# Kernel optimization log

Hardware: AMD Instinct MI355X
Metric: run time of the kernel (lower is better)

The kernel has to match this reference:

```python
import jax, jax.numpy as jnp
import numpy as np

S_Q = 2048; B = 2; H = 16; D = 128
SCALE = 1.0 / np.sqrt(128.0)  # softmax_scale from init


def setup_inputs() -> dict:
    key = jax.random.key(0)
    kq, kk, kv, ks = jax.random.split(key, 4)
    q = jax.random.normal(kq, (S_Q, B, H, D), dtype=jnp.float32)
    k = jax.random.normal(kk, (S_Q, B, 1, D), dtype=jnp.float32)   # MQA: H_kv=1
    v = jax.random.normal(kv, (S_Q, B, 1, D), dtype=jnp.float32)
    sinks = jax.random.normal(ks, (H,), dtype=jnp.float32)         # learned per-head sink logits
    return {"q": q, "k": k, "v": v, "sinks": sinks, "mask": 0}


def reference(q, k, v, sinks, mask):
    # q: [S_q, B, H, D]; k, v: [S_k, B, H_kv, D] (H_kv may be 1 -> MQA expand)
    S_q, Bn, Hq, Dn = q.shape
    S_k = k.shape[0]
    k = jnp.broadcast_to(k, (S_k, Bn, Hq, Dn))
    v = jnp.broadcast_to(v, (S_k, Bn, Hq, Dn))
    # logits: [B, H, S_q, S_k]
    logits = jnp.einsum("sbhd,tbhd->bhst", q.astype(jnp.float32), k.astype(jnp.float32)) * SCALE
    # causal mask (triu(-inf, diag=1) added in original)
    causal = jnp.tril(jnp.ones((S_q, S_k), dtype=bool))
    logits = jnp.where(causal[None, None], logits, -jnp.inf)
    # sink-augmented softmax: append sink logit as extra column, softmax, drop it
    sink = sinks.astype(jnp.float32)[None, :, None, None]        # [1, H, 1, 1]
    m = jax.lax.stop_gradient(jnp.maximum(logits.max(axis=-1, keepdims=True), sink))
    e = jnp.exp(logits - m)                                      # [B, H, S_q, S_k]
    denom = e.sum(axis=-1, keepdims=True) + jnp.exp(sink - m)    # sink column contribution
    probs = e / denom
    out = jnp.einsum("bhst,tbhd->sbhd", probs.astype(v.dtype), v)  # [S_q, B, H, D]
    return out.reshape(S_q, Bn, Hq * Dn)
```

## Files before the change

### kernel.cpp

```cpp
#include <hip/hip_runtime.h>
#include <hip/hip_bf16.h>

#define SQ 2048
#define NB 2
#define NH 16
#define DH 128
#define NKT 32
#define NQT 16
#define SCALE_L2E 0.1275174609f
#define LOG2E 1.4426950408889634f
#define DEFER_THR 11.0f

typedef _Float16 f16x8 __attribute__((ext_vector_type(8)));
typedef _Float16 f16x4 __attribute__((ext_vector_type(4)));
typedef __fp16 fp16x2 __attribute__((ext_vector_type(2)));
typedef float f32x4 __attribute__((ext_vector_type(4)));
typedef float f32x16 __attribute__((ext_vector_type(16)));
typedef unsigned int u32x4 __attribute__((ext_vector_type(4)));

static __device__ __forceinline__ _Float16 f2h(float f) { return (_Float16)f; }

static __device__ __forceinline__ unsigned int pkrtz(float a, float b) {
    fp16x2 h = __builtin_amdgcn_cvt_pkrtz(a, b);
    return __builtin_bit_cast(unsigned int, h);
}

__global__ __launch_bounds__(256)
void prepack(const float* __restrict__ k, const float* __restrict__ v,
             _Float16* __restrict__ kws, _Float16* __restrict__ vws) {
    const int tile  = blockIdx.x;
    const int which = tile >> 6;
    const int b     = (tile >> 5) & 1;
    const int kt    = tile & 31;
    const int tid   = threadIdx.x;

    if (which == 0) {
        const float* kbase = k + (size_t)kt * 64 * (NB * DH) + b * DH;
        _Float16* dst = kws + ((size_t)b * NKT + kt) * 8192;
        #pragma unroll
        for (int p = 0; p < 8; ++p) {
            const int id4 = tid + p * 256;
            const int row = id4 >> 5;
            const int c0  = (id4 & 31) << 2;
            f32x4 a = *(const f32x4*)(kbase + (size_t)row * (NB * DH) + c0);
            const int e = (row * 128 + c0) ^ ((row & 7) << 3);
            f16x4 pk = { f2h(a.x), f2h(a.y), f2h(a.z), f2h(a.w) };
            *(f16x4*)(dst + e) = pk;
        }
    } else {
        const float* vbase = v + b * DH;
        _Float16* dst = vws + ((size_t)b * NKT + kt) * 8192;
        const int d    = tid & 127;
        const int half = tid >> 7;
        #pragma unroll
        for (int p = 0; p < 8; ++p) {
            const int c0 = (p * 2 + half) * 4;
            float a0 = vbase[(size_t)(kt * 64 + c0 + 0) * (NB * DH) + d];
            float a1 = vbase[(size_t)(kt * 64 + c0 + 1) * (NB * DH) + d];
            float a2 = vbase[(size_t)(kt * 64 + c0 + 2) * (NB * DH) + d];
            float a3 = vbase[(size_t)(kt * 64 + c0 + 3) * (NB * DH) + d];
            const int e = (d * 64 + c0) ^ ((d & 7) << 3);
            f16x4 pk = { f2h(a0), f2h(a1), f2h(a2), f2h(a3) };
            *(f16x4*)(dst + e) = pk;
        }
    }
}

static __device__ __forceinline__ void gload16(const _Float16* gsrc, _Float16* ldst) {
    __builtin_amdgcn_global_load_lds(
        (const __attribute__((address_space(1))) void*)gsrc,
        (__attribute__((address_space(3))) void*)ldst, 16, 0, 0);
}

__global__ __launch_bounds__(256)
void attn_fwd(const float* __restrict__ q, const _Float16* __restrict__ kws,
              const _Float16* __restrict__ vws, const float* __restrict__ sinks,
              float* __restrict__ out) {
    __shared__ _Float16 Kb[2][8192];
    __shared__ _Float16 Vb[2][8192];

    const int tid  = threadIdx.x;
    const int w    = tid >> 6;
    const int lane = tid & 63;
    const int qc   = lane & 31;
    const int h2   = lane >> 5;

    const int bid  = blockIdx.x;
    const int b    = bid & 1;
    const int h    = (bid >> 1) & 15;
    const int slot = bid >> 5;
    const int qt   = (slot < 8) ? slot : 23 - slot;
    const int q0   = qt * 128;
    const int sq   = q0 + w * 32 + qc;

    f16x8 qf[8];
    {
        const float* qrow = q + ((size_t)sq * NB + b) * (NH * DH) + h * DH;
        #pragma unroll
        for (int ks = 0; ks < 8; ++ks) {
            const int d0 = ks * 16 + h2 * 8;
            f32x4 a = *(const f32x4*)(qrow + d0);
            f32x4 c = *(const f32x4*)(qrow + d0 + 4);
            f16x8 t;
            t[0] = f2h(a.x * SCALE_L2E); t[1] = f2h(a.y * SCALE_L2E);
            t[2] = f2h(a.z * SCALE_L2E); t[3] = f2h(a.w * SCALE_L2E);
            t[4] = f2h(c.x * SCALE_L2E); t[5] = f2h(c.y * SCALE_L2E);
            t[6] = f2h(c.z * SCALE_L2E); t[7] = f2h(c.w * SCALE_L2E);
            qf[ks] = t;
        }
    }

    float m_run = sinks[h] * LOG2E;
    float l_run = 1.0f;
    f32x16 acc[4];
    #pragma unroll
    for (int i = 0; i < 4; ++i) acc[i] = (f32x16)(0.0f);

    const _Float16* ktiles = kws + (size_t)b * NKT * 8192;
    const _Float16* vtiles = vws + (size_t)b * NKT * 8192;
    const int ntiles = 2 * qt + 2;

    #pragma unroll
    for (int j = 0; j < 4; ++j) {
        const int off = (w * 4 + j) * 512;
        gload16(ktiles + off + lane * 8, &Kb[0][off]);
        gload16(vtiles + off + lane * 8, &Vb[0][off]);
    }
    asm volatile("s_waitcnt vmcnt(0)" ::: "memory");
    __builtin_amdgcn_s_barrier();

    for (int it = 0; it < ntiles; ++it) {
        const int cur = it & 1;
        if (it + 1 < ntiles) {
            const _Float16* kt_n = ktiles + (size_t)(it + 1) * 8192;
            const _Float16* vt_n = vtiles + (size_t)(it + 1) * 8192;
            #pragma unroll
            for (int j = 0; j < 4; ++j) {
                const int off = (w * 4 + j) * 512;
                gload16(kt_n + off + lane * 8, &Kb[cur ^ 1][off]);
                gload16(vt_n + off + lane * 8, &Vb[cur ^ 1][off]);
            }
        }

        const int ktbase = it * 64;
        if (ktbase <= q0 + w * 32 + 31) {
            f32x16 sa0 = (f32x16)(0.0f), sa1 = (f32x16)(0.0f);
            __builtin_amdgcn_s_setprio(1);
            #pragma unroll
            for (int ks = 0; ks < 8; ++ks) {
                const int col = ks * 16 + h2 * 8;
                const int e0 = (qc * 128 + col) ^ ((qc & 7) << 3);
                const int e1 = ((32 + qc) * 128 + col) ^ ((qc & 7) << 3);
                f16x8 k0 = *(const f16x8*)(&Kb[cur][e0]);
                f16x8 k1 = *(const f16x8*)(&Kb[cur][e1]);
                sa0 = __builtin_amdgcn_mfma_f32_32x32x16_f16(k0, qf[ks], sa0, 0, 0, 0);
                sa1 = __builtin_amdgcn_mfma_f32_32x32x16_f16(k1, qf[ks], sa1, 0, 0, 0);
            }
            __builtin_amdgcn_s_setprio(0);

            float sv[32];
            #pragma unroll
            for (int i = 0; i < 16; ++i) { sv[i] = sa0[i]; sv[16 + i] = sa1[i]; }

            if (ktbase + 63 > q0 + w * 32) {
                #pragma unroll
                for (int mt = 0; mt < 2; ++mt)
                    #pragma unroll
                    for (int i = 0; i < 16; ++i) {
                        const int tk = ktbase + (i & 3) + 8 * (i >> 2) + 4 * h2 + 32 * mt;
                        if (tk > sq) sv[mt * 16 + i] = -1e30f;
                    }
            }

            float mx = sv[0];
            #pragma unroll
            for (int i = 1; i < 32; ++i) mx = fmaxf(mx, sv[i]);
            mx = fmaxf(mx, __shfl_xor(mx, 32));

            if (!__all(mx <= m_run + DEFER_THR)) {
                const float mnew = fmaxf(m_run, mx);
                const float corr = __builtin_amdgcn_exp2f(m_run - mnew);
                m_run = mnew;
                l_run *= corr;
                #pragma unroll
                for (int mt = 0; mt < 4; ++mt) acc[mt] *= corr;
            }

            float ls = 0.0f;
            #pragma unroll
            for (int i = 0; i < 32; ++i) {
                const float p = __builtin_amdgcn_exp2f(sv[i] - m_run);
                sv[i] = p;
                ls += p;
            }
            ls += __shfl_xor(ls, 32);
            l_run += ls;

            unsigned int pw[4][4];
            #pragma unroll
            for (int mt = 0; mt < 2; ++mt) {
                unsigned int e0[4], e1[4];
                #pragma unroll
                for (int bq = 0; bq < 4; ++bq) {
                    e0[bq] = pkrtz(sv[mt * 16 + 4 * bq + 0], sv[mt * 16 + 4 * bq + 1]);
                    e1[bq] = pkrtz(sv[mt * 16 + 4 * bq + 2], sv[mt * 16 + 4 * bq + 3]);
                }
                #pragma unroll
                for (int kl = 0; kl < 2; ++kl) {
                    unsigned int a0 = e0[2 * kl], b0 = e0[2 * kl + 1];
                    unsigned int a1 = e1[2 * kl], b1 = e1[2 * kl + 1];
                    asm volatile("v_permlane32_swap_b32 %0, %1" : "+v"(a0), "+v"(b0));
                    asm volatile("v_permlane32_swap_b32 %0, %1" : "+v"(a1), "+v"(b1));
                    pw[mt * 2 + kl][0] = a0; pw[mt * 2 + kl][1] = a1;
                    pw[mt * 2 + kl][2] = b0; pw[mt * 2 + kl][3] = b1;
                }
            }

            __builtin_amdgcn_s_setprio(1);
            #pragma unroll
            for (int ks = 0; ks < 4; ++ks) {
                u32x4 pu = { pw[ks][0], pw[ks][1], pw[ks][2], pw[ks][3] };
                f16x8 pf = __builtin_bit_cast(f16x8, pu);
                #pragma unroll
                for (int mt = 0; mt < 4; ++mt) {
                    const int d = mt * 32 + qc;
                    const int e = (d * 64 + ks * 16 + h2 * 8) ^ ((qc & 7) << 3);
                    f16x8 vf = *(const f16x8*)(&Vb[cur][e]);
                    acc[mt] = __builtin_amdgcn_mfma_f32_32x32x16_f16(vf, pf, acc[mt], 0, 0, 0);
                }
            }
            __builtin_amdgcn_s_setprio(0);
        }

        asm volatile("s_waitcnt vmcnt(0)" ::: "memory");
        __builtin_amdgcn_s_barrier();
    }

    const float rl = 1.0f / l_run;
    float* orow = out + ((size_t)sq * NB + b) * (NH * DH) + h * DH;
    #pragma unroll
    for (int mt = 0; mt < 4; ++mt)
        #pragma unroll
        for (int rg = 0; rg < 4; ++rg) {
            f32x4 o = { acc[mt][4 * rg + 0] * rl, acc[mt][4 * rg + 1] * rl,
                        acc[mt][4 * rg + 2] * rl, acc[mt][4 * rg + 3] * rl };
            *(f32x4*)(orow + mt * 32 + rg * 8 + h2 * 4) = o;
        }
}

extern "C" void kernel_launch(void* const* d_in, const int* in_sizes, int n_in,
                              void* d_out, int out_size, void* d_ws, size_t ws_size,
                              hipStream_t stream) {
    const float* q     = (const float*)d_in[0];
    const float* k     = (const float*)d_in[1];
    const float* v     = (const float*)d_in[2];
    const float* sinks = (const float*)d_in[3];
    float* out = (float*)d_out;

    _Float16* kws = (_Float16*)d_ws;
    _Float16* vws = kws + (size_t)NB * NKT * 8192;

    prepack<<<dim3(128), 256, 0, stream>>>(k, v, kws, vws);
    attn_fwd<<<dim3(NQT * NB * NH), 256, 0, stream>>>(q, kws, vws, sinks, out);
}
```

Measured before the change: 80.13 us.

## Single-buffer V tile loaded during QK, raise occupancy, reverse tile scheduling

V is now single-buffered and loaded for the current tile at the start of each iteration, overlapping its fetch with the QK^T and softmax phase, while K stays double-buffered. A mid-iteration partial vmcnt wait plus barrier separates the two phases. The smaller LDS footprint and a launch bound of 3 blocks per CU are meant to raise occupancy. The query-tile order is also reversed so the longest causal tiles launch first, at the cost of an extra barrier per iteration and V latency exposed if softmax is short.

```diff
diff --git a/kernel.cpp b/kernel.cpp
--- a/kernel.cpp
+++ b/kernel.cpp
@@ -1,5 +1,4 @@
 #include <hip/hip_runtime.h>
-#include <hip/hip_bf16.h>
 
 #define SQ 2048
 #define NB 2
@@ -72,12 +71,12 @@
         (__attribute__((address_space(3))) void*)ldst, 16, 0, 0);
 }
 
-__global__ __launch_bounds__(256)
+__global__ __launch_bounds__(256, 3)
 void attn_fwd(const float* __restrict__ q, const _Float16* __restrict__ kws,
               const _Float16* __restrict__ vws, const float* __restrict__ sinks,
               float* __restrict__ out) {
     __shared__ _Float16 Kb[2][8192];
-    __shared__ _Float16 Vb[2][8192];
+    __shared__ _Float16 Vb[8192];
 
     const int tid  = threadIdx.x;
     const int w    = tid >> 6;
@@ -89,7 +88,7 @@
     const int b    = bid & 1;
     const int h    = (bid >> 1) & 15;
     const int slot = bid >> 5;
-    const int qt   = (slot < 8) ? slot : 23 - slot;
+    const int qt   = (slot < 8) ? 15 - slot : slot - 8;
     const int q0   = qt * 128;
     const int sq   = q0 + w * 32 + qc;
 
@@ -119,31 +118,43 @@
     const _Float16* ktiles = kws + (size_t)b * NKT * 8192;
     const _Float16* vtiles = vws + (size_t)b * NKT * 8192;
     const int ntiles = 2 * qt + 2;
+    const int wlimit = q0 + w * 32 + 31;
 
     #pragma unroll
     for (int j = 0; j < 4; ++j) {
         const int off = (w * 4 + j) * 512;
         gload16(ktiles + off + lane * 8, &Kb[0][off]);
-        gload16(vtiles + off + lane * 8, &Vb[0][off]);
     }
     asm volatile("s_waitcnt vmcnt(0)" ::: "memory");
     __builtin_amdgcn_s_barrier();
+    asm volatile("" ::: "memory");
 
     for (int it = 0; it < ntiles; ++it) {
         const int cur = it & 1;
-        if (it + 1 < ntiles) {
-            const _Float16* kt_n = ktiles + (size_t)(it + 1) * 8192;
-            const _Float16* vt_n = vtiles + (size_t)(it + 1) * 8192;
+        const bool haveK = (it + 1 < ntiles);
+
+        {
+            const _Float16* vt = vtiles + (size_t)it * 8192;
             #pragma unroll
             for (int j = 0; j < 4; ++j) {
                 const int off = (w * 4 + j) * 512;
-                gload16(kt_n + off + lane * 8, &Kb[cur ^ 1][off]);
-                gload16(vt_n + off + lane * 8, &Vb[cur ^ 1][off]);
+                gload16(vt + off + lane * 8, &Vb[off]);
+            }
+        }
+        if (haveK) {
+            const _Float16* kn = ktiles + (size_t)(it + 1) * 8192;
+            #pragma unroll
+            for (int j = 0; j < 4; ++j) {
+                const int off = (w * 4 + j) * 512;
+                gload16(kn + off + lane * 8, &Kb[cur ^ 1][off]);
             }
         }
 
         const int ktbase = it * 64;
-        if (ktbase <= q0 + w * 32 + 31) {
+        const bool alive = (ktbase <= wlimit);
+        float sv[32];
+
+        if (alive) {
             f32x16 sa0 = (f32x16)(0.0f), sa1 = (f32x16)(0.0f);
             __builtin_amdgcn_s_setprio(1);
             #pragma unroll
@@ -158,7 +169,6 @@
             }
             __builtin_amdgcn_s_setprio(0);
 
-            float sv[32];
             #pragma unroll
             for (int i = 0; i < 16; ++i) { sv[i] = sa0[i]; sv[16 + i] = sa1[i]; }
 
@@ -195,7 +205,14 @@
             }
             ls += __shfl_xor(ls, 32);
             l_run += ls;
-
+        }
+
+        if (haveK) asm volatile("s_waitcnt vmcnt(4)" ::: "memory");
+        else       asm volatile("s_waitcnt vmcnt(0)" ::: "memory");
+        __builtin_amdgcn_s_barrier();
+        asm volatile("" ::: "memory");
+
+        if (alive) {
             unsigned int pw[4][4];
             #pragma unroll
             for (int mt = 0; mt < 2; ++mt) {
@@ -225,7 +242,7 @@
                 for (int mt = 0; mt < 4; ++mt) {
                     const int d = mt * 32 + qc;
                     const int e = (d * 64 + ks * 16 + h2 * 8) ^ ((qc & 7) << 3);
-                    f16x8 vf = *(const f16x8*)(&Vb[cur][e]);
+                    f16x8 vf = *(const f16x8*)(&Vb[e]);
                     acc[mt] = __builtin_amdgcn_mfma_f32_32x32x16_f16(vf, pf, acc[mt], 0, 0, 0);
                 }
             }
@@ -234,6 +251,7 @@
 
         asm volatile("s_waitcnt vmcnt(0)" ::: "memory");
         __builtin_amdgcn_s_barrier();
+        asm volatile("" ::: "memory");
     }
 
     const float rl = 1.0f / l_run;
```

Result: slower. 131.5 us (+64.1%).
